# Performance work log

Measured on AMD Instinct MI355X. Metric: run time of the kernel, lower is better.

## Reference

```python
import jax, jax.numpy as jnp
import numpy as np
import math

D = 512
B, L = 8, 2048
EPS = 1e-5

def setup_inputs() -> dict:
    key = jax.random.key(0)
    ks = jax.random.split(key, 8)
    s = 1.0 / math.sqrt(D)
    x = jax.random.normal(ks[0], (B, L, D), dtype=jnp.float32)
    adj = jax.random.randint(ks[1], (B, L, L), 0, 2, dtype=jnp.int32)
    Wq = jax.random.normal(ks[2], (D, D), dtype=jnp.float32) * s
    Wk = jax.random.normal(ks[3], (D, D), dtype=jnp.float32) * s
    Wv = jax.random.normal(ks[4], (D, D), dtype=jnp.float32) * s
    Wo = jax.random.normal(ks[5], (D, D), dtype=jnp.float32) * s
    bo = jnp.zeros((D,), dtype=jnp.float32)
    gamma = jnp.ones((D,), dtype=jnp.float32)
    beta = jnp.zeros((D,), dtype=jnp.float32)
    return {"x": x, "adj": adj, "Wq": Wq, "Wk": Wk, "Wv": Wv,
            "Wo": Wo, "bo": bo, "gamma": gamma, "beta": beta}

def layer_norm(y, gamma, beta):
    mu = jnp.mean(y, axis=-1, keepdims=True)
    var = jnp.mean(jnp.square(y - mu), axis=-1, keepdims=True)
    return (y - mu) * jax.lax.rsqrt(var + EPS) * gamma + beta

def reference(x, adj, Wq, Wk, Wv, Wo, bo, gamma, beta):
    d_out = Wq.shape[1]
    scale = 1.0 / math.sqrt(d_out)
    Q = x @ Wq                          # [B,L,D]
    K = x @ Wk
    V = x @ Wv
    sc = jnp.einsum('bld,bmd->blm', Q, K) * scale   # [B,L,L]
    mask = adj == 0
    sc = jnp.where(mask, -jnp.inf, sc)
    all_inf = jnp.all(mask, axis=-1, keepdims=True)  # rows with no neighbors
    sc = jnp.where(all_inf, 0.0, sc)                 # -> uniform attention
    w = jax.nn.softmax(sc, axis=-1)                  # dropout off (eval)
    out = jnp.einsum('blm,bmd->bld', w, V)
    y = x + out @ Wo + bo
    return layer_norm(y, gamma, beta)
```

## Files before the change

### kernel.cpp

```cpp
#include <hip/hip_runtime.h>
#include <hip/hip_bf16.h>

typedef short bf16x8 __attribute__((ext_vector_type(8)));
typedef float f32x4  __attribute__((ext_vector_type(4)));
typedef unsigned int u32;

#define LSEQ 2048
#define DDIM 512
#define NBAT 8

__device__ __forceinline__ void gld_lds16(const void* g, void* l) {
    __builtin_amdgcn_global_load_lds(
        (const __attribute__((address_space(1))) u32*)g,
        (__attribute__((address_space(3))) u32*)l, 16, 0, 0);
}
__device__ __forceinline__ float bf2f(short s) {
    u32 u = ((u32)(unsigned short)s) << 16;
    union { u32 u; float f; } c; c.u = u; return c.f;
}
__device__ __forceinline__ short f2bf(float f) {
    __hip_bfloat16 h = __float2bfloat16(f);
    return *(short*)&h;
}

__global__ void k_cvt(const float* __restrict__ x, const float* __restrict__ Wq,
                      const float* __restrict__ Wk, const float* __restrict__ Wv,
                      const float* __restrict__ Wo, __hip_bfloat16* __restrict__ xb,
                      __hip_bfloat16* __restrict__ Wtqkv, __hip_bfloat16* __restrict__ Wto) {
    __shared__ float t[32][33];
    if (blockIdx.x < 1024) {
        int mat = blockIdx.x >> 8;
        int tb  = blockIdx.x & 255;
        int tk  = tb >> 4, tn = tb & 15;
        const float* W = (mat == 0) ? Wq : (mat == 1) ? Wk : (mat == 2) ? Wv : Wo;
        int c  = threadIdx.x & 31;
        int r0 = threadIdx.x >> 5;
#pragma unroll
        for (int i = 0; i < 4; ++i) {
            int r = r0 + i * 8;
            t[r][c] = W[(size_t)(tk * 32 + r) * 512 + tn * 32 + c];
        }
        __syncthreads();
        __hip_bfloat16* dst = (mat < 3) ? (Wtqkv + (size_t)mat * 512 * 512) : Wto;
#pragma unroll
        for (int i = 0; i < 4; ++i) {
            int n = r0 + i * 8;
            dst[(size_t)(tn * 32 + n) * 512 + tk * 32 + c] = __float2bfloat16(t[c][n]);
        }
    } else {
        size_t i = ((size_t)(blockIdx.x - 1024) * 256 + threadIdx.x) * 4;
        float4 v = *(const float4*)(x + i);
        __hip_bfloat16 h[4] = { __float2bfloat16(v.x), __float2bfloat16(v.y),
                                __float2bfloat16(v.z), __float2bfloat16(v.w) };
        *(short4*)(xb + i) = *(short4*)h;
    }
}

__global__ __launch_bounds__(256, 2)
void k_gemm_qkv(const __hip_bfloat16* __restrict__ A, const __hip_bfloat16* __restrict__ Bt,
                __hip_bfloat16* __restrict__ Q, __hip_bfloat16* __restrict__ Kb,
                __hip_bfloat16* __restrict__ Vt) {
    __shared__ __hip_bfloat16 As[128][32], Bs[128][32];
    const int tid = threadIdx.x, lane = tid & 63, w = tid >> 6;
    const int l15 = lane & 15, l4 = lane >> 4;
    const int mt = blockIdx.x, nt = blockIdx.y;
    const int wr = (w >> 1) * 64, wc = (w & 1) * 64;
    const int sr = lane >> 2, so = (lane & 3) * 8;
    f32x4 acc[4][4] = {};

#pragma unroll 1
    for (int kt = 0; kt < 16; ++kt) {
        __syncthreads();
#pragma unroll
        for (int i = 0; i < 2; ++i) {
            int r0 = w * 32 + i * 16;
            gld_lds16(A  + (size_t)(mt * 128 + r0 + sr) * 512 + kt * 32 + so, &As[r0][0]);
            gld_lds16(Bt + (size_t)(nt * 128 + r0 + sr) * 512 + kt * 32 + so, &Bs[r0][0]);
        }
        __syncthreads();
        bf16x8 af[4], bfr[4];
#pragma unroll
        for (int i = 0; i < 4; ++i)
            af[i] = *(const bf16x8*)(&As[wr + 16 * i + l15][l4 * 8]);
#pragma unroll
        for (int j = 0; j < 4; ++j)
            bfr[j] = *(const bf16x8*)(&Bs[wc + 16 * j + l15][l4 * 8]);
        __builtin_amdgcn_s_setprio(1);
#pragma unroll
        for (int i = 0; i < 4; ++i)
#pragma unroll
            for (int j = 0; j < 4; ++j)
                acc[i][j] = __builtin_amdgcn_mfma_f32_16x16x32_bf16(af[i], bfr[j], acc[i][j], 0, 0, 0);
        __builtin_amdgcn_s_setprio(0);
    }
    const int which = (nt * 128) >> 9;
#pragma unroll
    for (int i = 0; i < 4; ++i) {
#pragma unroll
        for (int r = 0; r < 4; ++r) {
            int grow = mt * 128 + wr + 16 * i + (l4 << 2) + r;
#pragma unroll
            for (int j = 0; j < 4; ++j) {
                int gcol = nt * 128 + wc + 16 * j + l15;
                int cc = gcol & 511;
                __hip_bfloat16 h = __float2bfloat16(acc[i][j][r]);
                if (which == 0)      Q [(size_t)grow * 512 + cc] = h;
                else if (which == 1) Kb[(size_t)grow * 512 + cc] = h;
                else {
                    int b = grow >> 11, m = grow & 2047;
                    Vt[((size_t)b * 512 + cc) * 2048 + m] = h;
                }
            }
        }
    }
}

__global__ __launch_bounds__(512, 2)
void k_attn(const __hip_bfloat16* __restrict__ Q, const __hip_bfloat16* __restrict__ Kg,
            const __hip_bfloat16* __restrict__ Vt, const int* __restrict__ adj,
            __hip_bfloat16* __restrict__ P0, __hip_bfloat16* __restrict__ P1,
            float* __restrict__ mlb) {
    __shared__ __hip_bfloat16 Kl[2][32][520];
    __shared__ __hip_bfloat16 Vl[2][512][32];
    __shared__ __hip_bfloat16 Pl[8][16][40];
    const int tid = threadIdx.x, lane = tid & 63, w = tid >> 6;
    const int l15 = lane & 15, l4 = lane >> 4;
    const int b = blockIdx.x & 7, qt = (blockIdx.x >> 3) & 15, s = blockIdx.x >> 7;
    const float scale = 0.04419417382415922f;
    __hip_bfloat16* __restrict__ Op = s ? P1 : P0;

    const __hip_bfloat16* kbase = Kg + ((size_t)b * LSEQ + s * 1024) * 512;
    const __hip_bfloat16* vbase = Vt + (size_t)b * 512 * 2048 + s * 1024;
    const int* abase = adj + ((size_t)b * LSEQ + qt * 128 + w * 16 + l4 * 4) * LSEQ + s * 1024 + l15;
    const int vsr = lane >> 2;
    const int vswz = (l4 ^ ((l15 >> 1) & 3)) * 8;

    bf16x8 qf[16];
    {
        const __hip_bfloat16* qp = Q + ((size_t)b * LSEQ + qt * 128 + w * 16 + l15) * 512;
#pragma unroll
        for (int ks = 0; ks < 16; ++ks)
            qf[ks] = *(const bf16x8*)(qp + ks * 32 + l4 * 8);
    }
    f32x4 acc[32];
#pragma unroll
    for (int n = 0; n < 32; ++n) acc[n] = (f32x4){0.f, 0.f, 0.f, 0.f};
    float m_[4] = {-1e30f, -1e30f, -1e30f, -1e30f};
    float l_[4] = {0.f, 0.f, 0.f, 0.f};

    int adjv[8];
    {
#pragma unroll
        for (int i = 0; i < 4; ++i) {
            int r = w + i * 8;
            gld_lds16(kbase + (size_t)r * 512 + lane * 8, &Kl[0][r][0]);
        }
#pragma unroll
        for (int i = 0; i < 4; ++i) {
            int r0 = (w * 4 + i) * 16;
            int d  = r0 + vsr;
            gld_lds16(vbase + (size_t)d * 2048 + (((lane & 3) ^ ((d >> 1) & 3)) << 3), &Vl[0][r0][0]);
        }
#pragma unroll
        for (int r = 0; r < 4; ++r)
#pragma unroll
            for (int n = 0; n < 2; ++n)
                adjv[r * 2 + n] = abase[(size_t)r * LSEQ + n * 16];
    }
    __syncthreads();

#pragma unroll 1
    for (int t = 0; t < 32; ++t) {
        const int cur = t & 1, nxt = cur ^ 1;
        unsigned amask = 0;
#pragma unroll
        for (int r = 0; r < 4; ++r)
#pragma unroll
            for (int n = 0; n < 2; ++n)
                amask |= (adjv[r * 2 + n] != 0 ? 1u : 0u) << (n * 4 + r);
        if (t < 31) {
            const __hip_bfloat16* kp = kbase + (size_t)(t + 1) * 32 * 512;
#pragma unroll
            for (int i = 0; i < 4; ++i) {
                int r = w + i * 8;
                gld_lds16(kp + (size_t)r * 512 + lane * 8, &Kl[nxt][r][0]);
            }
            const __hip_bfloat16* vp = vbase + (t + 1) * 32;
#pragma unroll
            for (int i = 0; i < 4; ++i) {
                int r0 = (w * 4 + i) * 16;
                int d  = r0 + vsr;
                gld_lds16(vp + (size_t)d * 2048 + (((lane & 3) ^ ((d >> 1) & 3)) << 3), &Vl[nxt][r0][0]);
            }
            const int* ap = abase + (t + 1) * 32;
#pragma unroll
            for (int r = 0; r < 4; ++r)
#pragma unroll
                for (int n = 0; n < 2; ++n)
                    adjv[r * 2 + n] = ap[(size_t)r * LSEQ + n * 16];
        }
        f32x4 sa[2];
#pragma unroll
        for (int n = 0; n < 2; ++n) sa[n] = (f32x4){0.f, 0.f, 0.f, 0.f};
        __builtin_amdgcn_s_setprio(1);
#pragma unroll
        for (int ks = 0; ks < 16; ++ks) {
#pragma unroll
            for (int n = 0; n < 2; ++n) {
                bf16x8 bk = *(const bf16x8*)(&Kl[cur][n * 16 + l15][ks * 32 + l4 * 8]);
                sa[n] = __builtin_amdgcn_mfma_f32_16x16x32_bf16(qf[ks], bk, sa[n], 0, 0, 0);
            }
        }
        __builtin_amdgcn_s_setprio(0);
        float mx[4];
#pragma unroll
        for (int r = 0; r < 4; ++r) {
            float v = -1e30f;
#pragma unroll
            for (int n = 0; n < 2; ++n)
                if ((amask >> (n * 4 + r)) & 1) v = fmaxf(v, sa[n][r] * scale);
            v = fmaxf(v, __shfl_xor(v, 1));
            v = fmaxf(v, __shfl_xor(v, 2));
            v = fmaxf(v, __shfl_xor(v, 4));
            v = fmaxf(v, __shfl_xor(v, 8));
            mx[r] = v;
        }
        float rs[4];
        bool need = false;
#pragma unroll
        for (int r = 0; r < 4; ++r) {
            rs[r] = 1.f;
            if (mx[r] > m_[r] + 8.f) { rs[r] = __expf(m_[r] - mx[r]); m_[r] = mx[r]; }
            l_[r] *= rs[r];
            need |= (rs[r] != 1.f);
        }
        if (need) {
#pragma unroll
            for (int n = 0; n < 32; ++n) {
                acc[n][0] *= rs[0]; acc[n][1] *= rs[1];
                acc[n][2] *= rs[2]; acc[n][3] *= rs[3];
            }
        }
#pragma unroll
        for (int n = 0; n < 2; ++n)
#pragma unroll
            for (int r = 0; r < 4; ++r) {
                float p = ((amask >> (n * 4 + r)) & 1) ? __expf(sa[n][r] * scale - m_[r]) : 0.f;
                sa[n][r] = p;
            }
#pragma unroll
        for (int r = 0; r < 4; ++r) {
            float sm = sa[0][r] + sa[1][r];
            sm += __shfl_xor(sm, 1);
            sm += __shfl_xor(sm, 2);
            sm += __shfl_xor(sm, 4);
            sm += __shfl_xor(sm, 8);
            l_[r] += sm;
        }
#pragma unroll
        for (int n = 0; n < 2; ++n)
#pragma unroll
            for (int r = 0; r < 4; ++r)
                Pl[w][l4 * 4 + r][n * 16 + l15] = __float2bfloat16(sa[n][r]);
        {
            bf16x8 pf = *(const bf16x8*)(&Pl[w][l15][l4 * 8]);
            __builtin_amdgcn_s_setprio(1);
#pragma unroll
            for (int n = 0; n < 32; ++n) {
                bf16x8 bv = *(const bf16x8*)(&Vl[cur][n * 16 + l15][vswz]);
                acc[n] = __builtin_amdgcn_mfma_f32_16x16x32_bf16(pf, bv, acc[n], 0, 0, 0);
            }
            __builtin_amdgcn_s_setprio(0);
        }
        __syncthreads();
    }
#pragma unroll
    for (int r = 0; r < 4; ++r) {
        size_t row = (size_t)b * LSEQ + qt * 128 + w * 16 + l4 * 4 + r;
#pragma unroll
        for (int n = 0; n < 32; ++n)
            Op[row * 512 + n * 16 + l15] = __float2bfloat16(acc[n][r]);
        if (l15 == 0) {
            mlb[((size_t)s * 16384 + row) * 2 + 0] = m_[r];
            mlb[((size_t)s * 16384 + row) * 2 + 1] = l_[r];
        }
    }
}

__global__ __launch_bounds__(512, 2)
void k_out_ln(const __hip_bfloat16* __restrict__ p0, const __hip_bfloat16* __restrict__ p1,
              const float* __restrict__ mlb, const __hip_bfloat16* __restrict__ Bt,
              const float* __restrict__ x, const float* __restrict__ bo,
              const float* __restrict__ gamma, const float* __restrict__ beta,
              float* __restrict__ out) {
    __shared__ __hip_bfloat16 As[64][32];
    __shared__ __hip_bfloat16 Bs[512][32];
    __shared__ float part[64][4][2];
    __shared__ float lnmv[64][2];
    const int tid = threadIdx.x, lane = tid & 63, w = tid >> 6;
    const int l15 = lane & 15, l4 = lane >> 4;
    const int mt = blockIdx.x;
    const int rs = (w >> 2) * 32, cbs = (w & 3) * 128;
    f32x4 acc[2][8] = {};

    float c0 = 0.f, c1 = 0.f;
    size_t grow_s = 0;
    int ko = (tid & 3) * 8;
    if (tid < 256) {
        int arow = tid >> 2;
        grow_s = (size_t)mt * 64 + arow;
        float m0 = mlb[grow_s * 2], l0 = mlb[grow_s * 2 + 1];
        float m1 = mlb[(16384 + grow_s) * 2], l1 = mlb[(16384 + grow_s) * 2 + 1];
        float M  = fmaxf(m0, m1);
        float e0 = __expf(m0 - M), e1 = __expf(m1 - M);
        float den = l0 * e0 + l1 * e1;
        float inv = (den > 0.f) ? 1.f / den : 0.f;
        c0 = e0 * inv; c1 = e1 * inv;
    }

#pragma unroll 1
    for (int kt = 0; kt < 16; ++kt) {
        __syncthreads();
#pragma unroll
        for (int i = 0; i < 4; ++i) {
            int br = w * 64 + i * 16;
            gld_lds16(Bt + (size_t)(br + (lane >> 2)) * 512 + kt * 32 + (lane & 3) * 8, &Bs[br][0]);
        }
        if (tid < 256) {
            bf16x8 a0 = *(const bf16x8*)(p0 + grow_s * 512 + kt * 32 + ko);
            bf16x8 a1 = *(const bf16x8*)(p1 + grow_s * 512 + kt * 32 + ko);
            short h[8];
#pragma unroll
            for (int k = 0; k < 8; ++k)
                h[k] = f2bf(c0 * bf2f(a0[k]) + c1 * bf2f(a1[k]));
            *(bf16x8*)(&As[tid >> 2][ko]) = *(bf16x8*)h;
        }
        __syncthreads();
        bf16x8 af[2], bfr[8];
#pragma unroll
        for (int i = 0; i < 2; ++i)
            af[i] = *(const bf16x8*)(&As[rs + 16 * i + l15][l4 * 8]);
#pragma unroll
        for (int j = 0; j < 8; ++j)
            bfr[j] = *(const bf16x8*)(&Bs[cbs + 16 * j + l15][l4 * 8]);
        __builtin_amdgcn_s_setprio(1);
#pragma unroll
        for (int i = 0; i < 2; ++i)
#pragma unroll
            for (int j = 0; j < 8; ++j)
                acc[i][j] = __builtin_amdgcn_mfma_f32_16x16x32_bf16(af[i], bfr[j], acc[i][j], 0, 0, 0);
        __builtin_amdgcn_s_setprio(0);
    }
#pragma unroll
    for (int i = 0; i < 2; ++i) {
#pragma unroll
        for (int r = 0; r < 4; ++r) {
            int rl = rs + 16 * i + 4 * l4 + r;
            size_t grow = (size_t)mt * 64 + rl;
            float s = 0.f, q = 0.f;
#pragma unroll
            for (int j = 0; j < 8; ++j) {
                int col = cbs + 16 * j + l15;
                float y = x[grow * 512 + col] + acc[i][j][r] + bo[col];
                acc[i][j][r] = y;
                s += y; q += y * y;
            }
            s += __shfl_xor(s, 1); q += __shfl_xor(q, 1);
            s += __shfl_xor(s, 2); q += __shfl_xor(q, 2);
            s += __shfl_xor(s, 4); q += __shfl_xor(q, 4);
            s += __shfl_xor(s, 8); q += __shfl_xor(q, 8);
            if (l15 == 0) { part[rl][w & 3][0] = s; part[rl][w & 3][1] = q; }
        }
    }
    __syncthreads();
    if (tid < 64) {
        float S  = part[tid][0][0] + part[tid][1][0] + part[tid][2][0] + part[tid][3][0];
        float Q2 = part[tid][0][1] + part[tid][1][1] + part[tid][2][1] + part[tid][3][1];
        float mu = S * (1.f / 512.f);
        float var = Q2 * (1.f / 512.f) - mu * mu;
        lnmv[tid][0] = mu;
        lnmv[tid][1] = rsqrtf(var + 1e-5f);
    }
    __syncthreads();
    float gm[8], bt2[8];
#pragma unroll
    for (int j = 0; j < 8; ++j) {
        int col = cbs + 16 * j + l15;
        gm[j] = gamma[col]; bt2[j] = beta[col];
    }
#pragma unroll
    for (int i = 0; i < 2; ++i) {
#pragma unroll
        for (int r = 0; r < 4; ++r) {
            int rl = rs + 16 * i + 4 * l4 + r;
            size_t grow = (size_t)mt * 64 + rl;
            float mu = lnmv[rl][0], rsd = lnmv[rl][1];
#pragma unroll
            for (int j = 0; j < 8; ++j) {
                int col = cbs + 16 * j + l15;
                out[grow * 512 + col] = (acc[i][j][r] - mu) * rsd * gm[j] + bt2[j];
            }
        }
    }
}

extern "C" void kernel_launch(void* const* d_in, const int* in_sizes, int n_in,
                              void* d_out, int out_size, void* d_ws, size_t ws_size,
                              hipStream_t stream) {
    const float* x     = (const float*)d_in[0];
    const int*   adj   = (const int*)d_in[1];
    const float* Wq    = (const float*)d_in[2];
    const float* Wk    = (const float*)d_in[3];
    const float* Wv    = (const float*)d_in[4];
    const float* Wo    = (const float*)d_in[5];
    const float* bo    = (const float*)d_in[6];
    const float* gamma = (const float*)d_in[7];
    const float* beta  = (const float*)d_in[8];
    float* out = (float*)d_out;

    char* ws = (char*)d_ws;
    const size_t SZ_ROWS = (size_t)NBAT * LSEQ;
    __hip_bfloat16* xb    = (__hip_bfloat16*)(ws);
    __hip_bfloat16* Wtqkv = (__hip_bfloat16*)(ws + 16777216);
    __hip_bfloat16* Wto   = (__hip_bfloat16*)(ws + 18350080);
    __hip_bfloat16* Qb    = (__hip_bfloat16*)(ws + 18874368);
    __hip_bfloat16* Kb    = (__hip_bfloat16*)(ws + 35651584);
    __hip_bfloat16* Vtb   = (__hip_bfloat16*)(ws + 52428800);
    __hip_bfloat16* P1    = (__hip_bfloat16*)(ws + 69206016);
    float*          mlb   = (float*)         (ws + 85983232);
    __hip_bfloat16* P0    = xb;
    (void)in_sizes; (void)n_in; (void)out_size; (void)ws_size;

    k_cvt<<<1024 + (unsigned)((SZ_ROWS * DDIM) / (256 * 4)), 256, 0, stream>>>(
        x, Wq, Wk, Wv, Wo, xb, Wtqkv, Wto);
    k_gemm_qkv<<<dim3(128, 12), 256, 0, stream>>>(xb, Wtqkv, Qb, Kb, Vtb);
    k_attn<<<256, 512, 0, stream>>>(Qb, Kb, Vtb, adj, P0, P1, mlb);
    k_out_ln<<<256, 512, 0, stream>>>(P0, P1, mlb, Wto, x, bo, gamma, beta, out);
}
```

Before: 236.3 us.

## Restructure attention PV step so each wave owns a 64-column slice of D

The attention kernel now processes 64 keys per iteration instead of 32. Softmax probabilities for all 128 query rows and their rescale factors are shared through LDS, and each wave computes P·V for all rows but only its own 64 output columns. This removes per-wave redundant reads of the full V tile and the conditional accumulator rescale. In exchange, K/V double buffering is dropped in favour of single buffers with extra barriers, which exposes load latency. Adjacency loads are no longer prefetched ahead of use.

```diff
diff --git a/kernel.cpp b/kernel.cpp
--- a/kernel.cpp
+++ b/kernel.cpp
@@ -120,9 +120,10 @@
             const __hip_bfloat16* __restrict__ Vt, const int* __restrict__ adj,
             __hip_bfloat16* __restrict__ P0, __hip_bfloat16* __restrict__ P1,
             float* __restrict__ mlb) {
-    __shared__ __hip_bfloat16 Kl[2][32][520];
-    __shared__ __hip_bfloat16 Vl[2][512][32];
-    __shared__ __hip_bfloat16 Pl[8][16][40];
+    __shared__ __hip_bfloat16 Kl[64][520];
+    __shared__ __hip_bfloat16 Vl[512 * 64];
+    __shared__ __hip_bfloat16 Ps[128][72];
+    __shared__ float rsl[128];
     const int tid = threadIdx.x, lane = tid & 63, w = tid >> 6;
     const int l15 = lane & 15, l4 = lane >> 4;
     const int b = blockIdx.x & 7, qt = (blockIdx.x >> 3) & 15, s = blockIdx.x >> 7;
@@ -132,8 +133,8 @@
     const __hip_bfloat16* kbase = Kg + ((size_t)b * LSEQ + s * 1024) * 512;
     const __hip_bfloat16* vbase = Vt + (size_t)b * 512 * 2048 + s * 1024;
     const int* abase = adj + ((size_t)b * LSEQ + qt * 128 + w * 16 + l4 * 4) * LSEQ + s * 1024 + l15;
-    const int vsr = lane >> 2;
-    const int vswz = (l4 ^ ((l15 >> 1) & 3)) * 8;
+    const int vrw = lane >> 3;
+    const int vln = ((lane & 7) ^ vrw) * 8;
 
     bf16x8 qf[16];
     {
@@ -142,72 +143,44 @@
         for (int ks = 0; ks < 16; ++ks)
             qf[ks] = *(const bf16x8*)(qp + ks * 32 + l4 * 8);
     }
-    f32x4 acc[32];
-#pragma unroll
-    for (int n = 0; n < 32; ++n) acc[n] = (f32x4){0.f, 0.f, 0.f, 0.f};
+    f32x4 acc[8][4] = {};
     float m_[4] = {-1e30f, -1e30f, -1e30f, -1e30f};
     float l_[4] = {0.f, 0.f, 0.f, 0.f};
 
-    int adjv[8];
     {
 #pragma unroll
-        for (int i = 0; i < 4; ++i) {
-            int r = w + i * 8;
-            gld_lds16(kbase + (size_t)r * 512 + lane * 8, &Kl[0][r][0]);
-        }
-#pragma unroll
-        for (int i = 0; i < 4; ++i) {
-            int r0 = (w * 4 + i) * 16;
-            int d  = r0 + vsr;
-            gld_lds16(vbase + (size_t)d * 2048 + (((lane & 3) ^ ((d >> 1) & 3)) << 3), &Vl[0][r0][0]);
-        }
-#pragma unroll
-        for (int r = 0; r < 4; ++r)
-#pragma unroll
-            for (int n = 0; n < 2; ++n)
-                adjv[r * 2 + n] = abase[(size_t)r * LSEQ + n * 16];
+        for (int i = 0; i < 8; ++i) {
+            int r = w * 8 + i;
+            gld_lds16(kbase + (size_t)r * 512 + lane * 8, &Kl[r][0]);
+        }
+#pragma unroll
+        for (int i = 0; i < 8; ++i) {
+            int d0 = (w * 8 + i) * 8;
+            gld_lds16(vbase + (size_t)(d0 + vrw) * 2048 + vln, &Vl[d0 * 64]);
+        }
     }
     __syncthreads();
 
 #pragma unroll 1
-    for (int t = 0; t < 32; ++t) {
-        const int cur = t & 1, nxt = cur ^ 1;
+    for (int t = 0; t < 16; ++t) {
         unsigned amask = 0;
-#pragma unroll
-        for (int r = 0; r < 4; ++r)
-#pragma unroll
-            for (int n = 0; n < 2; ++n)
-                amask |= (adjv[r * 2 + n] != 0 ? 1u : 0u) << (n * 4 + r);
-        if (t < 31) {
-            const __hip_bfloat16* kp = kbase + (size_t)(t + 1) * 32 * 512;
-#pragma unroll
-            for (int i = 0; i < 4; ++i) {
-                int r = w + i * 8;
-                gld_lds16(kp + (size_t)r * 512 + lane * 8, &Kl[nxt][r][0]);
-            }
-            const __hip_bfloat16* vp = vbase + (t + 1) * 32;
-#pragma unroll
-            for (int i = 0; i < 4; ++i) {
-                int r0 = (w * 4 + i) * 16;
-                int d  = r0 + vsr;
-                gld_lds16(vp + (size_t)d * 2048 + (((lane & 3) ^ ((d >> 1) & 3)) << 3), &Vl[nxt][r0][0]);
-            }
-            const int* ap = abase + (t + 1) * 32;
+        {
+            const int* ap = abase + t * 64;
 #pragma unroll
             for (int r = 0; r < 4; ++r)
 #pragma unroll
-                for (int n = 0; n < 2; ++n)
-                    adjv[r * 2 + n] = ap[(size_t)r * LSEQ + n * 16];
-        }
-        f32x4 sa[2];
-#pragma unroll
-        for (int n = 0; n < 2; ++n) sa[n] = (f32x4){0.f, 0.f, 0.f, 0.f};
+                for (int n = 0; n < 4; ++n)
+                    amask |= (ap[(size_t)r * LSEQ + n * 16] != 0 ? 1u : 0u) << (n * 4 + r);
+        }
+        f32x4 sa[4];
+#pragma unroll
+        for (int n = 0; n < 4; ++n) sa[n] = (f32x4){0.f, 0.f, 0.f, 0.f};
         __builtin_amdgcn_s_setprio(1);
 #pragma unroll
         for (int ks = 0; ks < 16; ++ks) {
 #pragma unroll
-            for (int n = 0; n < 2; ++n) {
-                bf16x8 bk = *(const bf16x8*)(&Kl[cur][n * 16 + l15][ks * 32 + l4 * 8]);
+            for (int n = 0; n < 4; ++n) {
+                bf16x8 bk = *(const bf16x8*)(&Kl[n * 16 + l15][ks * 32 + l4 * 8]);
                 sa[n] = __builtin_amdgcn_mfma_f32_16x16x32_bf16(qf[ks], bk, sa[n], 0, 0, 0);
             }
         }
@@ -217,7 +190,7 @@
         for (int r = 0; r < 4; ++r) {
             float v = -1e30f;
 #pragma unroll
-            for (int n = 0; n < 2; ++n)
+            for (int n = 0; n < 4; ++n)
                 if ((amask >> (n * 4 + r)) & 1) v = fmaxf(v, sa[n][r] * scale);
             v = fmaxf(v, __shfl_xor(v, 1));
             v = fmaxf(v, __shfl_xor(v, 2));
@@ -226,61 +199,88 @@
             mx[r] = v;
         }
         float rs[4];
-        bool need = false;
 #pragma unroll
         for (int r = 0; r < 4; ++r) {
             rs[r] = 1.f;
             if (mx[r] > m_[r] + 8.f) { rs[r] = __expf(m_[r] - mx[r]); m_[r] = mx[r]; }
             l_[r] *= rs[r];
-            need |= (rs[r] != 1.f);
-        }
-        if (need) {
-#pragma unroll
-            for (int n = 0; n < 32; ++n) {
-                acc[n][0] *= rs[0]; acc[n][1] *= rs[1];
-                acc[n][2] *= rs[2]; acc[n][3] *= rs[3];
-            }
-        }
-#pragma unroll
-        for (int n = 0; n < 2; ++n)
+        }
+#pragma unroll
+        for (int n = 0; n < 4; ++n)
 #pragma unroll
             for (int r = 0; r < 4; ++r) {
                 float p = ((amask >> (n * 4 + r)) & 1) ? __expf(sa[n][r] * scale - m_[r]) : 0.f;
                 sa[n][r] = p;
-            }
-#pragma unroll
-        for (int r = 0; r < 4; ++r) {
-            float sm = sa[0][r] + sa[1][r];
+                Ps[w * 16 + l4 * 4 + r][n * 16 + l15] = __float2bfloat16(p);
+            }
+#pragma unroll
+        for (int r = 0; r < 4; ++r) {
+            float sm = sa[0][r] + sa[1][r] + sa[2][r] + sa[3][r];
             sm += __shfl_xor(sm, 1);
             sm += __shfl_xor(sm, 2);
             sm += __shfl_xor(sm, 4);
             sm += __shfl_xor(sm, 8);
             l_[r] += sm;
         }
-#pragma unroll
-        for (int n = 0; n < 2; ++n)
-#pragma unroll
-            for (int r = 0; r < 4; ++r)
-                Pl[w][l4 * 4 + r][n * 16 + l15] = __float2bfloat16(sa[n][r]);
-        {
-            bf16x8 pf = *(const bf16x8*)(&Pl[w][l15][l4 * 8]);
-            __builtin_amdgcn_s_setprio(1);
-#pragma unroll
-            for (int n = 0; n < 32; ++n) {
-                bf16x8 bv = *(const bf16x8*)(&Vl[cur][n * 16 + l15][vswz]);
-                acc[n] = __builtin_amdgcn_mfma_f32_16x16x32_bf16(pf, bv, acc[n], 0, 0, 0);
-            }
-            __builtin_amdgcn_s_setprio(0);
-        }
-        __syncthreads();
-    }
-#pragma unroll
-    for (int r = 0; r < 4; ++r) {
-        size_t row = (size_t)b * LSEQ + qt * 128 + w * 16 + l4 * 4 + r;
-#pragma unroll
-        for (int n = 0; n < 32; ++n)
-            Op[row * 512 + n * 16 + l15] = __float2bfloat16(acc[n][r]);
         if (l15 == 0) {
+#pragma unroll
+            for (int r = 0; r < 4; ++r) rsl[w * 16 + l4 * 4 + r] = rs[r];
+        }
+        __syncthreads();
+        if (t < 15) {
+            const __hip_bfloat16* kp = kbase + (size_t)(t + 1) * 64 * 512;
+#pragma unroll
+            for (int i = 0; i < 8; ++i) {
+                int r = w * 8 + i;
+                gld_lds16(kp + (size_t)r * 512 + lane * 8, &Kl[r][0]);
+            }
+        }
+        bf16x8 vf[8];
+#pragma unroll
+        for (int n = 0; n < 4; ++n)
+#pragma unroll
+            for (int ks2 = 0; ks2 < 2; ++ks2)
+                vf[n * 2 + ks2] = *(const bf16x8*)(
+                    &Vl[(w * 64 + n * 16 + l15) * 64 + (((ks2 * 4 + l4) ^ (l15 & 7)) << 3)]);
+        __builtin_amdgcn_s_setprio(1);
+#pragma unroll
+        for (int m = 0; m < 8; ++m) {
+            f32x4 rw = *(const f32x4*)(&rsl[m * 16 + l4 * 4]);
+            bf16x8 pf0 = *(const bf16x8*)(&Ps[m * 16 + l15][l4 * 8]);
+            bf16x8 pf1 = *(const bf16x8*)(&Ps[m * 16 + l15][32 + l4 * 8]);
+#pragma unroll
+            for (int n = 0; n < 4; ++n) {
+                acc[m][n] = acc[m][n] * rw;
+                acc[m][n] = __builtin_amdgcn_mfma_f32_16x16x32_bf16(pf0, vf[n * 2], acc[m][n], 0, 0, 0);
+                acc[m][n] = __builtin_amdgcn_mfma_f32_16x16x32_bf16(pf1, vf[n * 2 + 1], acc[m][n], 0, 0, 0);
+            }
+        }
+        __builtin_amdgcn_s_setprio(0);
+        __syncthreads();
+        if (t < 15) {
+            const __hip_bfloat16* vp = vbase + (t + 1) * 64;
+#pragma unroll
+            for (int i = 0; i < 8; ++i) {
+                int d0 = (w * 8 + i) * 8;
+                gld_lds16(vp + (size_t)(d0 + vrw) * 2048 + vln, &Vl[d0 * 64]);
+            }
+        }
+        __syncthreads();
+    }
+#pragma unroll
+    for (int m = 0; m < 8; ++m) {
+#pragma unroll
+        for (int r = 0; r < 4; ++r) {
+            size_t row = (size_t)b * LSEQ + qt * 128 + m * 16 + l4 * 4 + r;
+#pragma unroll
+            for (int n = 0; n < 4; ++n)
+                Op[row * 512 + w * 64 + n * 16 + l15] = __float2bfloat16(acc[m][n][r]);
+        }
+    }
+    if (l15 == 0) {
+#pragma unroll
+        for (int r = 0; r < 4; ++r) {
+            size_t row = (size_t)b * LSEQ + qt * 128 + w * 16 + l4 * 4 + r;
             mlb[((size_t)s * 16384 + row) * 2 + 0] = m_[r];
             mlb[((size_t)s * 16384 + row) * 2 + 1] = l_[r];
         }
@@ -332,7 +332,7 @@
             short h[8];
 #pragma unroll
             for (int k = 0; k < 8; ++k)
-                h[k] = f2bf(c0 * bf2f(a0[k]) + c1 * bf2f(a1[k]));
+                h[k] = f2bf(c0 * bf2f(((short*)&a0)[k]) + c1 * bf2f(((short*)&a1)[k]));
             *(bf16x8*)(&As[tid >> 2][ko]) = *(bf16x8*)h;
         }
         __syncthreads();
```

Measured after the change: 373.4 us. 58.0% more time.
